# Kernel optimization log

Hardware: AMD Instinct MI355X
Metric: run time of the kernel (lower is better)

## Reference

```python
import jax, jax.numpy as jnp
import numpy as np

N_HEADS = 16

def setup_inputs() -> dict:
    key = jax.random.key(0)
    qkv = jax.random.normal(key, (4, 3072, 2048), dtype=jnp.float32)
    return {"qkv": qkv}

def reference(qkv) -> jnp.ndarray:
    bs, width, length = qkv.shape
    ch = width // (3 * N_HEADS)
    # [bs*H, 3*ch, T] -> split into q, k, v each [bs*H, ch, T]
    qkv_r = qkv.reshape(bs * N_HEADS, 3 * ch, length)
    q, k, v = qkv_r[:, :ch], qkv_r[:, ch:2 * ch], qkv_r[:, 2 * ch:]
    scale = 1.0 / jnp.sqrt(jnp.sqrt(jnp.float32(ch)))
    # scores: [bs*H, T, T]
    weight = jnp.einsum('bct,bcs->bts', q * scale, k * scale)
    weight = jax.nn.softmax(weight.astype(jnp.float32), axis=-1).astype(weight.dtype)
    a = jnp.einsum('bts,bcs->bct', weight, v)  # [bs*H, ch, T]
    return a.reshape(bs, N_HEADS * ch, length)
```

## Files before the change

kernel.cpp:

```cpp
#include <hip/hip_runtime.h>

namespace {

constexpr int D  = 64;
constexpr int T  = 2048;
constexpr int NT = T / 64;
constexpr float SCL = 0.125f * 1.44269504088896340736f;

constexpr size_t QP_OFF  = (size_t)64 * 32 * 8192;
constexpr size_t WS_NEED = ((size_t)64 * 32 * 8192 + (size_t)64 * 32 * 4096) * 2;

typedef __bf16 bf16x8 __attribute__((ext_vector_type(8)));
typedef float  f32x4  __attribute__((ext_vector_type(4)));
typedef unsigned short u16x4 __attribute__((ext_vector_type(4)));
typedef unsigned short u16x8 __attribute__((ext_vector_type(8)));
typedef unsigned int   u32x2 __attribute__((ext_vector_type(2)));
typedef short          s16x4 __attribute__((ext_vector_type(4)));

__device__ inline unsigned short f2bf(float f) {
    unsigned int u = __builtin_bit_cast(unsigned int, f);
    u += 0x7FFFu + ((u >> 16) & 1u);
    return (unsigned short)(u >> 16);
}

__device__ inline unsigned int pkbf(float a, float b) {
#if __has_builtin(__builtin_amdgcn_cvt_pk_bf16_f32)
    auto r = __builtin_amdgcn_cvt_pk_bf16_f32(a, b);
    static_assert(sizeof(r) == 4, "cvt_pk_bf16 size");
    return __builtin_bit_cast(unsigned int, r);
#else
    return (unsigned int)f2bf(a) | ((unsigned int)f2bf(b) << 16);
#endif
}

__device__ inline int frag_off(int row, int c0) {
    int g = (c0 >> 3) ^ ((row >> 1) & 7);
    return row * 64 + g * 8;
}

__device__ inline void async_cp16(const void* g, void* l) {
    __builtin_amdgcn_global_load_lds(
        (const __attribute__((address_space(1))) unsigned int*)g,
        (__attribute__((address_space(3))) unsigned int*)l, 16, 0, 0);
}

__global__ __launch_bounds__(256)
void prepass(const float* __restrict__ qkv, unsigned short* __restrict__ ws) {
    const int tile = blockIdx.x, h = blockIdx.y, z = blockIdx.z;
    const int tid = threadIdx.x;
    const float* src = qkv + (size_t)h * 3 * D * T + (size_t)z * D * T + tile * 64;
    __shared__ unsigned short L[4096];

    if (z == 2) {
        unsigned short* dst = ws + (size_t)(h * 32 + tile) * 8192 + 4096;
        const int c = tid >> 2, g = tid & 3;
        const int sg = g ^ ((c >> 2) & 3);
        #pragma unroll
        for (int wq = 0; wq < 4; wq++) {
            f32x4 a = *(const f32x4*)(src + (size_t)c * T + wq * 16 + sg * 4);
            u16x4 wv = { f2bf(a[0]), f2bf(a[1]), f2bf(a[2]), f2bf(a[3]) };
            *(u16x4*)(dst + wq * 1024 + tid * 4) = wv;
        }
    } else {
        const float m = (z == 0) ? SCL : 1.0f;
        const int c0 = (tid >> 4) * 4, s4 = tid & 15;
        float fr[4][4];
        #pragma unroll
        for (int r = 0; r < 4; r++)
            *(f32x4*)fr[r] = *(const f32x4*)(src + (size_t)(c0 + r) * T + s4 * 4);
        #pragma unroll
        for (int j = 0; j < 4; j++) {
            int trow = s4 * 4 + j;
            u16x4 wv = { f2bf(fr[0][j] * m), f2bf(fr[1][j] * m),
                         f2bf(fr[2][j] * m), f2bf(fr[3][j] * m) };
            *(u16x4*)(L + frag_off(trow, c0) + (c0 & 7)) = wv;
        }
        __syncthreads();
        unsigned short* dst = (z == 0)
            ? ws + QP_OFF + (size_t)(h * 32 + tile) * 4096
            : ws + (size_t)(h * 32 + tile) * 8192;
        #pragma unroll
        for (int i = 0; i < 2; i++)
            *(u16x8*)(dst + tid * 16 + i * 8) = *(const u16x8*)(L + tid * 16 + i * 8);
    }
}


#define STAGE(J, B)                                                          \
  { const char* g = kvb + (size_t)(J) * 16384;                               \
    char* lk = lbase + (B) * 16384;                                          \
    async_cp16(g,         lk);                                               \
    async_cp16(g + 4096,  lk + 4096);                                        \
    async_cp16(g + 8192,  lk + 8192);                                        \
    async_cp16(g + 12288, lk + 12288); }

#define BODY(KT, B, DO_STAGE, WAITIMM)                                       \
  {                                                                          \
    __builtin_amdgcn_s_waitcnt(WAITIMM);         \
    __builtin_amdgcn_s_barrier();             \
    __builtin_amdgcn_sched_barrier(0);          \
    _Pragma("unroll")                                                        \
    for (int q = 0; q < 4; q++) {                                            \
      const char* kb = sbuf + (B) * 16384 + q * 2048;                        \
      const char* vb = sbuf + (B) * 16384 + 8192 + q * 2048;                 \
      bf16x8 aK0 = *(const bf16x8*)(kb + aK0o);                              \
      bf16x8 aK1 = *(const bf16x8*)(kb + aK1o);                              \
      s16x4 aV0 = *(const s16x4*)(vb + aVo);                                 \
      s16x4 aV1 = *(const s16x4*)(vb + aVo + 512);                           \
      s16x4 aV2 = *(const s16x4*)(vb + aVo + 1024);                          \
      s16x4 aV3 = *(const s16x4*)(vb + aVo + 1536);                          \
      _Pragma("unroll")                                                      \
      for (int st = 0; st < 2; st++) {                                       \
        f32x4 s = __builtin_amdgcn_mfma_f32_16x16x32_bf16(                   \
            aK0, bQ[st][0], ZF, 0, 0, 0);                                    \
        s = __builtin_amdgcn_mfma_f32_16x16x32_bf16(aK1, bQ[st][1], s, 0,0,0);\
        float p0 = __builtin_amdgcn_exp2f(s[0]);                             \
        float p1 = __builtin_amdgcn_exp2f(s[1]);                             \
        float p2 = __builtin_amdgcn_exp2f(s[2]);                             \
        float p3 = __builtin_amdgcn_exp2f(s[3]);                             \
        l_acc[st] += (p0 + p1) + (p2 + p3);                                  \
        u32x2 pk = { pkbf(p0, p1), pkbf(p2, p3) };                           \
        s16x4 bP = __builtin_bit_cast(s16x4, pk);                            \
        acc_o[st][0] = __builtin_amdgcn_mfma_f32_16x16x16bf16_1k(            \
            aV0, bP, acc_o[st][0], 0, 0, 0);                                 \
        acc_o[st][1] = __builtin_amdgcn_mfma_f32_16x16x16bf16_1k(            \
            aV1, bP, acc_o[st][1], 0, 0, 0);                                 \
        acc_o[st][2] = __builtin_amdgcn_mfma_f32_16x16x16bf16_1k(            \
            aV2, bP, acc_o[st][2], 0, 0, 0);                                 \
        acc_o[st][3] = __builtin_amdgcn_mfma_f32_16x16x16bf16_1k(            \
            aV3, bP, acc_o[st][3], 0, 0, 0);                                 \
      }                                                                      \
    }                                                                        \
    if (DO_STAGE) {                                                          \
      __builtin_amdgcn_s_waitcnt(0xC07F);        \
      __builtin_amdgcn_s_barrier();           \
      STAGE((KT) + 2, B)                                                     \
    }                                                                        \
  }

__global__ __launch_bounds__(256, 4)
void attn_main(const unsigned short* __restrict__ ws, float* __restrict__ out) {
    const int h  = blockIdx.x;
    const int qt = blockIdx.y;
    const int t0 = qt * 128;
    const int tid  = threadIdx.x;
    const int lane = tid & 63;
    const int w    = tid >> 6;
    const int ln   = lane & 15, q4 = lane >> 4;

    __shared__ char sbuf[32768];
    char* lbase = sbuf + w * 1024;

    const int aK0o = 2 * frag_off(ln, q4 * 8);
    const int aK1o = 2 * frag_off(ln, 32 + q4 * 8);
    const int aVo  = 32 * ln + 2 * ((q4 ^ ((ln >> 2) & 3)) * 4);

    const unsigned short* qtile = ws + QP_OFF + (size_t)(h * 32 + qt * 2) * 4096;
    bf16x8 bQ[2][2];
    #pragma unroll
    for (int st = 0; st < 2; st++) {
        bQ[st][0] = *(const bf16x8*)(qtile + st * 4096 + frag_off(16 * w + ln, q4 * 8));
        bQ[st][1] = *(const bf16x8*)(qtile + st * 4096 + frag_off(16 * w + ln, 32 + q4 * 8));
    }

    const char* kvb = (const char*)ws + (size_t)(h * 32) * 16384
                      + w * 1024 + lane * 16;
    STAGE(0, 0)
    STAGE(1, 1)

    const f32x4 ZF = {0.f, 0.f, 0.f, 0.f};
    f32x4 acc_o[2][4];
    #pragma unroll
    for (int st = 0; st < 2; st++)
        #pragma unroll
        for (int ci = 0; ci < 4; ci++) acc_o[st][ci] = ZF;
    float l_acc[2] = {0.f, 0.f};

    #pragma unroll 1
    for (int m = 0; m < 15; m++) {
        BODY(2 * m,     0, 1, 0x0F74)
        BODY(2 * m + 1, 1, 1, 0x0F74)
    }
    BODY(30, 0, 0, 0x0F74)
    BODY(31, 1, 0, 0x0F70)

    #pragma unroll
    for (int st = 0; st < 2; st++) {
        float sl = l_acc[st];
        sl += __shfl_xor(sl, 16, 64);
        sl += __shfl_xor(sl, 32, 64);
        const float linv = 1.0f / sl;
        float* ob = out + (size_t)h * D * T + t0 + st * 64 + 16 * w + ln;
        #pragma unroll
        for (int ci = 0; ci < 4; ci++)
            #pragma unroll
            for (int rr = 0; rr < 4; rr++)
                ob[(size_t)(16 * ci + q4 * 4 + rr) * T] = acc_o[st][ci][rr] * linv;
    }
}

__device__ inline bf16x8 frag8(const unsigned short* p, int row, int c0) {
    return *(const bf16x8*)(p + frag_off(row, c0));
}

__global__ __launch_bounds__(256)
void attn_fallback(const float* __restrict__ qkv, float* __restrict__ out) {
    const int h     = blockIdx.y;
    const int t0    = blockIdx.x * 64;
    const int tid   = threadIdx.x;
    const int lane  = tid & 63;
    const int strip = tid >> 6;
    const int ln    = lane & 15;
    const int q4    = lane >> 4;

    __shared__ unsigned short Qs[64 * D];
    __shared__ unsigned short Ks[64 * D];
    __shared__ unsigned short Vs[D * 64];
    __shared__ unsigned short Pss[64 * 64];
    __shared__ float l_lds[64];

    const float* qb = qkv + (size_t)h * 3 * D * T;
    const float* kb = qb + (size_t)D * T;
    const float* vb = qb + (size_t)(2 * D) * T;
    const int s4 = tid & 15;
    const int c0 = (tid >> 4) * 4;
    {
        float fr[4][4];
        #pragma unroll
        for (int r = 0; r < 4; r++)
            *(f32x4*)fr[r] = *(const f32x4*)(qb + (size_t)(c0 + r) * T + t0 + s4 * 4);
        #pragma unroll
        for (int j = 0; j < 4; j++) {
            int trow = s4 * 4 + j;
            u16x4 wv = { f2bf(fr[0][j]), f2bf(fr[1][j]), f2bf(fr[2][j]), f2bf(fr[3][j]) };
            *(u16x4*)(Qs + frag_off(trow, c0) + (c0 & 7)) = wv;
        }
    }
    __syncthreads();
    const int arow = strip * 16 + ln;
    const int kg   = q4 * 8;
    const bf16x8 aq0 = frag8(Qs, arow, kg);
    const bf16x8 aq1 = frag8(Qs, arow, 32 + kg);
    f32x4 acc_o[4];
    #pragma unroll
    for (int m = 0; m < 4; m++) acc_o[m] = (f32x4){0.f, 0.f, 0.f, 0.f};
    float l_acc[4] = {0.f, 0.f, 0.f, 0.f};
    constexpr float S2 = 0.125f * 1.44269504088896340736f;
    for (int kt = 0; kt < NT; kt++) {
        const int s0 = kt * 64;
        float kr[4][4], vr[4][4];
        #pragma unroll
        for (int r = 0; r < 4; r++)
            *(f32x4*)kr[r] = *(const f32x4*)(kb + (size_t)(c0 + r) * T + s0 + s4 * 4);
        #pragma unroll
        for (int r = 0; r < 4; r++)
            *(f32x4*)vr[r] = *(const f32x4*)(vb + (size_t)(c0 + r) * T + s0 + s4 * 4);
        __syncthreads();
        #pragma unroll
        for (int j = 0; j < 4; j++) {
            int srow = s4 * 4 + j;
            u16x4 wk = { f2bf(kr[0][j]), f2bf(kr[1][j]), f2bf(kr[2][j]), f2bf(kr[3][j]) };
            *(u16x4*)(Ks + frag_off(srow, c0) + (c0 & 7)) = wk;
        }
        #pragma unroll
        for (int r = 0; r < 4; r++) {
            int row = c0 + r, cc = s4 * 4;
            u16x4 wv = { f2bf(vr[r][0]), f2bf(vr[r][1]), f2bf(vr[r][2]), f2bf(vr[r][3]) };
            *(u16x4*)(Vs + frag_off(row, cc) + (cc & 7)) = wv;
        }
        __syncthreads();
        f32x4 accs[4];
        #pragma unroll
        for (int ns = 0; ns < 4; ns++) {
            bf16x8 b0 = frag8(Ks, ns * 16 + ln, kg);
            bf16x8 b1 = frag8(Ks, ns * 16 + ln, 32 + kg);
            f32x4 z = {0.f, 0.f, 0.f, 0.f};
            z = __builtin_amdgcn_mfma_f32_16x16x32_bf16(aq0, b0, z, 0, 0, 0);
            z = __builtin_amdgcn_mfma_f32_16x16x32_bf16(aq1, b1, z, 0, 0, 0);
            accs[ns] = z;
        }
        #pragma unroll
        for (int ns = 0; ns < 4; ns++) {
            int scol = ns * 16 + ln;
            #pragma unroll
            for (int r = 0; r < 4; r++) {
                float p = __builtin_amdgcn_exp2f(accs[ns][r] * S2);
                l_acc[r] += p;
                int trow = strip * 16 + q4 * 4 + r;
                int g = ((scol >> 3) ^ ((trow >> 1) & 7));
                Pss[trow * 64 + g * 8 + (scol & 7)] = f2bf(p);
            }
        }
        bf16x8 bp0 = frag8(Pss, arow, kg);
        bf16x8 bp1 = frag8(Pss, arow, 32 + kg);
        #pragma unroll
        for (int ms = 0; ms < 4; ms++) {
            bf16x8 av0 = frag8(Vs, ms * 16 + ln, kg);
            bf16x8 av1 = frag8(Vs, ms * 16 + ln, 32 + kg);
            acc_o[ms] = __builtin_amdgcn_mfma_f32_16x16x32_bf16(av0, bp0, acc_o[ms], 0, 0, 0);
            acc_o[ms] = __builtin_amdgcn_mfma_f32_16x16x32_bf16(av1, bp1, acc_o[ms], 0, 0, 0);
        }
    }
    #pragma unroll
    for (int r = 0; r < 4; r++) {
        float s = l_acc[r];
        s += __shfl_xor(s, 1, 64);
        s += __shfl_xor(s, 2, 64);
        s += __shfl_xor(s, 4, 64);
        s += __shfl_xor(s, 8, 64);
        if (ln == 0) l_lds[strip * 16 + q4 * 4 + r] = s;
    }
    const float linv = 1.0f / l_lds[strip * 16 + ln];
    const int tg = t0 + strip * 16 + ln;
    float* ob = out + (size_t)h * D * T;
    #pragma unroll
    for (int ms = 0; ms < 4; ms++)
        #pragma unroll
        for (int r = 0; r < 4; r++) {
            int c = ms * 16 + q4 * 4 + r;
            ob[(size_t)c * T + tg] = acc_o[ms][r] * linv;
        }
}

}

extern "C" void kernel_launch(void* const* d_in, const int* in_sizes, int n_in,
                              void* d_out, int out_size, void* d_ws, size_t ws_size,
                              hipStream_t stream) {
    const float* qkv = (const float*)d_in[0];
    float* out = (float*)d_out;
    if (ws_size >= WS_NEED) {
        prepass<<<dim3(32, 64, 3), 256, 0, stream>>>(qkv, (unsigned short*)d_ws);
        attn_main<<<dim3(64, 16), 256, 0, stream>>>((const unsigned short*)d_ws, out);
    } else {
        attn_fallback<<<dim3(32, 64), 256, 0, stream>>>(qkv, out);
    }
}
```

Measured before the change: 247.2 us.

## Split each KV tile across two wave groups and merge partial outputs

Doubles the attention block from 256 to 512 threads. Two groups of four waves each process half of every 64-key tile while sharing the same query rows, and all 512 threads cooperatively stage K/V with fewer async copies per thread. The partial output accumulators and row sums are merged through shared memory before normalisation and the store. The aim is more waves per block to hide MFMA and exp latency. It adds an LDS reduction and extra barriers at the end, and occupancy now depends on the new launch bounds.

```diff
diff --git a/kernel.cpp b/kernel.cpp
--- a/kernel.cpp
+++ b/kernel.cpp
@@ -89,10 +89,8 @@
 #define STAGE(J, B)                                                          \
   { const char* g = kvb + (size_t)(J) * 16384;                               \
     char* lk = lbase + (B) * 16384;                                          \
-    async_cp16(g,         lk);                                               \
-    async_cp16(g + 4096,  lk + 4096);                                        \
-    async_cp16(g + 8192,  lk + 8192);                                        \
-    async_cp16(g + 12288, lk + 12288); }
+    async_cp16(g,        lk);                                                \
+    async_cp16(g + 8192, lk + 8192); }
 
 #define BODY(KT, B, DO_STAGE, WAITIMM)                                       \
   {                                                                          \
@@ -100,9 +98,9 @@
     __builtin_amdgcn_s_barrier();             \
     __builtin_amdgcn_sched_barrier(0);          \
     _Pragma("unroll")                                                        \
-    for (int q = 0; q < 4; q++) {                                            \
-      const char* kb = sbuf + (B) * 16384 + q * 2048;                        \
-      const char* vb = sbuf + (B) * 16384 + 8192 + q * 2048;                 \
+    for (int qq = 0; qq < 2; qq++) {          \
+      const char* kb = sbuf + (B) * 16384 + qBase + qq * 2048;               \
+      const char* vb = kb + 8192;                                            \
       bf16x8 aK0 = *(const bf16x8*)(kb + aK0o);                              \
       bf16x8 aK1 = *(const bf16x8*)(kb + aK1o);                              \
       s16x4 aV0 = *(const s16x4*)(vb + aVo);                                 \
@@ -138,7 +136,7 @@
     }                                                                        \
   }
 
-__global__ __launch_bounds__(256, 4)
+__global__ __launch_bounds__(512, 6)
 void attn_main(const unsigned short* __restrict__ ws, float* __restrict__ out) {
     const int h  = blockIdx.x;
     const int qt = blockIdx.y;
@@ -146,11 +144,15 @@
     const int tid  = threadIdx.x;
     const int lane = tid & 63;
     const int w    = tid >> 6;
+    const int sg   = w >> 2;
+    const int ts   = w & 3;
     const int ln   = lane & 15, q4 = lane >> 4;
 
-    __shared__ char sbuf[32768];
-    char* lbase = sbuf + w * 1024;
-
+    __shared__ char  sbuf[32768];
+    __shared__ float lmrg[128];
+    char* lbase = sbuf + tid * 16;
+
+    const int qBase = sg * 4096;
     const int aK0o = 2 * frag_off(ln, q4 * 8);
     const int aK1o = 2 * frag_off(ln, 32 + q4 * 8);
     const int aVo  = 32 * ln + 2 * ((q4 ^ ((ln >> 2) & 3)) * 4);
@@ -159,12 +161,11 @@
     bf16x8 bQ[2][2];
     #pragma unroll
     for (int st = 0; st < 2; st++) {
-        bQ[st][0] = *(const bf16x8*)(qtile + st * 4096 + frag_off(16 * w + ln, q4 * 8));
-        bQ[st][1] = *(const bf16x8*)(qtile + st * 4096 + frag_off(16 * w + ln, 32 + q4 * 8));
-    }
-
-    const char* kvb = (const char*)ws + (size_t)(h * 32) * 16384
-                      + w * 1024 + lane * 16;
+        bQ[st][0] = *(const bf16x8*)(qtile + st * 4096 + frag_off(16 * ts + ln, q4 * 8));
+        bQ[st][1] = *(const bf16x8*)(qtile + st * 4096 + frag_off(16 * ts + ln, 32 + q4 * 8));
+    }
+
+    const char* kvb = (const char*)ws + (size_t)(h * 32) * 16384 + tid * 16;
     STAGE(0, 0)
     STAGE(1, 1)
 
@@ -178,24 +179,47 @@
 
     #pragma unroll 1
     for (int m = 0; m < 15; m++) {
-        BODY(2 * m,     0, 1, 0x0F74)
-        BODY(2 * m + 1, 1, 1, 0x0F74)
-    }
-    BODY(30, 0, 0, 0x0F74)
+        BODY(2 * m,     0, 1, 0x0F72)
+        BODY(2 * m + 1, 1, 1, 0x0F72)
+    }
+    BODY(30, 0, 0, 0x0F72)
     BODY(31, 1, 0, 0x0F70)
 
+    float lg[2];
     #pragma unroll
     for (int st = 0; st < 2; st++) {
-        float sl = l_acc[st];
-        sl += __shfl_xor(sl, 16, 64);
-        sl += __shfl_xor(sl, 32, 64);
-        const float linv = 1.0f / sl;
-        float* ob = out + (size_t)h * D * T + t0 + st * 64 + 16 * w + ln;
-        #pragma unroll
-        for (int ci = 0; ci < 4; ci++)
+        float s = l_acc[st];
+        s += __shfl_xor(s, 16, 64);
+        s += __shfl_xor(s, 32, 64);
+        lg[st] = s;
+    }
+    __syncthreads();
+    float* slots = (float*)sbuf;
+    if (sg == 1) {
+        #pragma unroll
+        for (int st = 0; st < 2; st++) {
+            float* dst = slots + (ts * 2 + st) * 1024;
             #pragma unroll
-            for (int rr = 0; rr < 4; rr++)
-                ob[(size_t)(16 * ci + q4 * 4 + rr) * T] = acc_o[st][ci][rr] * linv;
+            for (int ci = 0; ci < 4; ci++)
+                *(f32x4*)(dst + ci * 256 + lane * 4) = acc_o[st][ci];
+            if (q4 == 0) lmrg[(ts * 2 + st) * 16 + ln] = lg[st];
+        }
+    }
+    __syncthreads();
+    if (sg == 0) {
+        #pragma unroll
+        for (int st = 0; st < 2; st++) {
+            const float* srcp = slots + (ts * 2 + st) * 1024;
+            const float linv = 1.0f / (lg[st] + lmrg[(ts * 2 + st) * 16 + ln]);
+            float* ob = out + (size_t)h * D * T + t0 + st * 64 + 16 * ts + ln;
+            #pragma unroll
+            for (int ci = 0; ci < 4; ci++) {
+                f32x4 v = acc_o[st][ci] + *(const f32x4*)(srcp + ci * 256 + lane * 4);
+                #pragma unroll
+                for (int rr = 0; rr < 4; rr++)
+                    ob[(size_t)(16 * ci + q4 * 4 + rr) * T] = v[rr] * linv;
+            }
+        }
     }
 }
 
@@ -331,7 +355,7 @@
     float* out = (float*)d_out;
     if (ws_size >= WS_NEED) {
         prepass<<<dim3(32, 64, 3), 256, 0, stream>>>(qkv, (unsigned short*)d_ws);
-        attn_main<<<dim3(64, 16), 256, 0, stream>>>((const unsigned short*)d_ws, out);
+        attn_main<<<dim3(64, 16), 512, 0, stream>>>((const unsigned short*)d_ws, out);
     } else {
         attn_fallback<<<dim3(32, 64), 256, 0, stream>>>(qkv, out);
     }
```

Result: slower. 788.7 us (+219.1%).
